# Optimization experiments

Hardware: AMD Instinct MI355X
Metric: run time of the kernel (lower is better)

The kernel has to match this reference:

```python
import jax, jax.numpy as jnp
import numpy as np

D = 2048
H = 16
HD = D // H
DFF = 8192
EPS = 1e-6


def rmsnorm(x, w):
    xf = x.astype(jnp.float32)
    var = jnp.mean(xf * xf, axis=-1, keepdims=True)
    return w * (xf * jax.lax.rsqrt(var + EPS)).astype(x.dtype)


def setup_inputs() -> dict:
    key = jax.random.key(0)
    ks = jax.random.split(key, 10)
    s = 0.02
    return {
        "hidden_states": jax.random.normal(ks[0], (2, 2048, D), jnp.float32),
        "wq": jax.random.normal(ks[1], (D, D), jnp.float32) * s,
        "wk": jax.random.normal(ks[2], (D, D), jnp.float32) * s,
        "wv": jax.random.normal(ks[3], (D, D), jnp.float32) * s,
        "wo": jax.random.normal(ks[4], (D, D), jnp.float32) * s,
        "w_gate": jax.random.normal(ks[5], (DFF, D), jnp.float32) * s,
        "w_up": jax.random.normal(ks[6], (DFF, D), jnp.float32) * s,
        "w_down": jax.random.normal(ks[7], (D, DFF), jnp.float32) * s,
        "ln1_w": jnp.ones((D,), jnp.float32),
        "ln2_w": jnp.ones((D,), jnp.float32),
    }


def reference(hidden_states, wq, wk, wv, wo, w_gate, w_up, w_down, ln1_w, ln2_w):
    B, S, _ = hidden_states.shape
    residual = hidden_states
    x = rmsnorm(hidden_states, ln1_w)
    # projections (torch Linear: y = x @ W.T), split heads -> [B,H,S,HD]
    q = (x @ wq.T).reshape(B, S, H, HD).transpose(0, 2, 1, 3)
    k = (x @ wk.T).reshape(B, S, H, HD).transpose(0, 2, 1, 3)
    v = (x @ wv.T).reshape(B, S, H, HD).transpose(0, 2, 1, 3)
    scores = jnp.einsum("bhqd,bhkd->bhqk", q, k) / np.sqrt(HD).astype(np.float32)
    causal = jnp.triu(jnp.ones((S, S), bool), k=1)  # True above diagonal -> masked
    scores = jnp.where(causal, -jnp.inf, scores)
    attn = jax.nn.softmax(scores, axis=-1)
    out = jnp.einsum("bhqk,bhkd->bhqd", attn, v)
    out = out.transpose(0, 2, 1, 3).reshape(B, S, D)
    out = out @ wo.T
    hidden = residual + out
    residual = hidden
    y = rmsnorm(hidden, ln2_w)
    gate = y @ w_gate.T
    up = y @ w_up.T
    mlp = (jax.nn.silu(gate) * up) @ w_down.T
    return residual + mlp
```

## Files before the change

kernel.cpp:

```cpp
#include <hip/hip_runtime.h>
#include <stdint.h>

#define D_MODEL 2048
#define NHEADS  16
#define HEADDIM 128
#define DFF     8192
#define BATCH   2
#define SEQ     2048
#define NTOK    (BATCH*SEQ)
#define EPS     1e-6f
#define QKV_RS  (3*D_MODEL)

typedef unsigned short u16;
typedef short  s16x8 __attribute__((ext_vector_type(8)));
typedef float  f32x4 __attribute__((ext_vector_type(4)));

__device__ __forceinline__ u16 f2bf(float f) {
  union { float f; uint32_t u; } v; v.f = f;
  uint32_t u = v.u;
  return (u16)((u + 0x7fffu + ((u >> 16) & 1u)) >> 16);
}
__device__ __forceinline__ float bf2f(u16 h) {
  union { uint32_t u; float f; } v; v.u = ((uint32_t)h) << 16;
  return v.f;
}

__device__ __forceinline__ void gload_lds16(const void* g, void* l) {
  __builtin_amdgcn_global_load_lds(
      (const __attribute__((address_space(1))) void*)g,
      (__attribute__((address_space(3))) void*)l, 16, 0, 0);
}

__device__ __forceinline__ f32x4 mfma16(s16x8 a, s16x8 b, f32x4 c) {
  return __builtin_amdgcn_mfma_f32_16x16x32_bf16(a, b, c, 0, 0, 0);
}

#define BAR()   asm volatile("s_barrier" ::: "memory")
#define LGK0()  asm volatile("s_waitcnt lgkmcnt(0)" ::: "memory")

__device__ __forceinline__ void cvt_one(const float* in, u16* out, int i) {
  float4 v = ((const float4*)in)[i];
  uint32_t lo = (uint32_t)f2bf(v.x) | ((uint32_t)f2bf(v.y) << 16);
  uint32_t hi = (uint32_t)f2bf(v.z) | ((uint32_t)f2bf(v.w) << 16);
  uint2 st; st.x = lo; st.y = hi;
  ((uint2*)out)[i] = st;
}

__global__ __launch_bounds__(256)
void cvt_kernel(const float* __restrict__ in, u16* __restrict__ out, int n4)
{
  int idx = blockIdx.x * 256 + threadIdx.x;
  int stride = gridDim.x * 256;
  for (int i = idx; i < n4; i += stride) cvt_one(in, out, i);
}

__global__ __launch_bounds__(256)
void cvt4_kernel(const float* __restrict__ a, const float* __restrict__ b,
                 const float* __restrict__ c, const float* __restrict__ d,
                 u16* __restrict__ oa, u16* __restrict__ ob,
                 u16* __restrict__ oc, u16* __restrict__ od, int n4)
{
  int idx = blockIdx.x * 256 + threadIdx.x;
  int stride = gridDim.x * 256;
  for (int i = idx; i < 4 * n4; i += stride) {
    int w = i / n4, j = i - w * n4;
    const float* s = (w == 0) ? a : (w == 1) ? b : (w == 2) ? c : d;
    u16* o = (w == 0) ? oa : (w == 1) ? ob : (w == 2) ? oc : od;
    cvt_one(s, o, j);
  }
}

__global__ __launch_bounds__(256)
void cvt2_kernel(const float* __restrict__ a, const float* __restrict__ b,
                 u16* __restrict__ oa, u16* __restrict__ ob, int n4)
{
  int idx = blockIdx.x * 256 + threadIdx.x;
  int stride = gridDim.x * 256;
  for (int i = idx; i < 2 * n4; i += stride) {
    int w = i / n4, j = i - w * n4;
    cvt_one(w ? b : a, w ? ob : oa, j);
  }
}

__global__ __launch_bounds__(256)
void rmsnorm_kernel(const float* __restrict__ x, const float* __restrict__ w,
                    u16* __restrict__ out)
{
  int row = blockIdx.x;
  int tid = threadIdx.x;
  const float4* xr = (const float4*)(x + (size_t)row * D_MODEL);
  float4 a = xr[tid];
  float4 b = xr[tid + 256];
  float ss = a.x*a.x + a.y*a.y + a.z*a.z + a.w*a.w
           + b.x*b.x + b.y*b.y + b.z*b.z + b.w*b.w;
#pragma unroll
  for (int o = 32; o > 0; o >>= 1) ss += __shfl_xor(ss, o);
  __shared__ float red[4];
  if ((tid & 63) == 0) red[tid >> 6] = ss;
  __syncthreads();
  float tot = red[0] + red[1] + red[2] + red[3];
  float sc = rsqrtf(tot * (1.0f / D_MODEL) + EPS);
  const float4* wr = (const float4*)w;
  float4 wa = wr[tid], wb = wr[tid + 256];
  u16* orow = out + (size_t)row * D_MODEL;
  uint2 s0, s1;
  s0.x = (uint32_t)f2bf(a.x*wa.x*sc) | ((uint32_t)f2bf(a.y*wa.y*sc) << 16);
  s0.y = (uint32_t)f2bf(a.z*wa.z*sc) | ((uint32_t)f2bf(a.w*wa.w*sc) << 16);
  s1.x = (uint32_t)f2bf(b.x*wb.x*sc) | ((uint32_t)f2bf(b.y*wb.y*sc) << 16);
  s1.y = (uint32_t)f2bf(b.z*wb.z*sc) | ((uint32_t)f2bf(b.w*wb.w*sc) << 16);
  ((uint2*)orow)[tid] = s0;
  ((uint2*)orow)[tid + 256] = s1;
}

#define BM 128
#define BN 128
#define BK 64

template<int EPI>
__global__ __launch_bounds__(256, 2)
void gemm_bt(const u16* __restrict__ A, const u16* __restrict__ B,
             void* __restrict__ Cout, const float* __restrict__ aux,
             int M, int N, int K)
{
  __shared__ u16 As[BM * BK];
  __shared__ u16 Bs[BN * BK];
  const int nbn = N / BN;
  int bid = blockIdx.x;
  int swz = (gridDim.x & 7) ? bid : ((bid & 7) * (gridDim.x >> 3) + (bid >> 3));
  const int bm = swz / nbn, bn = swz % nbn;
  const int m0 = bm * BM, n0 = bn * BN;
  const int tid = threadIdx.x;
  const int lane = tid & 63;
  const int wm = tid >> 7, wn = (tid >> 6) & 1;
  const int lr = lane & 15, lg = lane >> 4;

  f32x4 acc[4][4] = {};

  for (int k0 = 0; k0 < K; k0 += BK) {
#pragma unroll
    for (int i = 0; i < 4; ++i) {
      int c = i * 256 + tid;
      int row = c >> 3, cr = c & 7;
      int g = cr ^ (row & 7);
      gload_lds16(A + (size_t)(m0 + row) * K + k0 + (g << 3), &As[c * 8]);
      gload_lds16(B + (size_t)(n0 + row) * K + k0 + (g << 3), &Bs[c * 8]);
    }
    __syncthreads();
#pragma unroll
    for (int kk = 0; kk < BK; kk += 32) {
      s16x8 a[4], b[4];
#pragma unroll
      for (int m = 0; m < 4; ++m) {
        int row = wm * 64 + m * 16 + lr;
        int j = (kk >> 3) + lg;
        a[m] = *(const s16x8*)&As[row * BK + ((j ^ (row & 7)) << 3)];
      }
#pragma unroll
      for (int n = 0; n < 4; ++n) {
        int row = wn * 64 + n * 16 + lr;
        int j = (kk >> 3) + lg;
        b[n] = *(const s16x8*)&Bs[row * BK + ((j ^ (row & 7)) << 3)];
      }
#pragma unroll
      for (int m = 0; m < 4; ++m)
#pragma unroll
        for (int n = 0; n < 4; ++n)
          acc[m][n] = mfma16(a[m], b[n], acc[m][n]);
    }
    __syncthreads();
  }

#pragma unroll
  for (int m = 0; m < 4; ++m) {
#pragma unroll
    for (int n = 0; n < 4; ++n) {
      int col = n0 + wn * 64 + n * 16 + lr;
#pragma unroll
      for (int r = 0; r < 4; ++r) {
        int row = m0 + wm * 64 + m * 16 + lg * 4 + r;
        size_t idx = (size_t)row * N + col;
        float v = acc[m][n][r];
        if (EPI == 0) {
          ((u16*)Cout)[idx] = f2bf(v);
        } else if (EPI == 1) {
          float up = bf2f(((u16*)Cout)[idx]);
          float s = v / (1.0f + __expf(-v));
          ((u16*)Cout)[idx] = f2bf(s * up);
        } else if (EPI == 2) {
          ((float*)Cout)[idx] = aux[idx] + v;
        } else {
          ((float*)Cout)[idx] += v;
        }
      }
    }
  }
}

template<int EPI>
__global__ __launch_bounds__(512, 2)
void gemm256(const u16* __restrict__ A, const u16* __restrict__ B,
             void* __restrict__ Cout, const float* __restrict__ aux,
             int M, int N, int K)
{
  __shared__ u16 As[2][2][256 * 32];
  __shared__ u16 Bs[2][2][256 * 32];
  const int nbn = N >> 8;
  const int bm = blockIdx.x / nbn, bn = blockIdx.x % nbn;
  const int m0 = bm << 8, n0 = bn << 8;
  const int tid = threadIdx.x, lane = tid & 63;
  const int wid = tid >> 6;
  const int wm = wid >> 2, wn = wid & 3;
  const int lr = lane & 15, lg = lane >> 4;

  f32x4 acc[8][4] = {};

  auto stA = [&](int t, int kh) {
    const u16* src = A + (size_t)m0 * K + t * 64 + kh * 32;
    u16* dst = &As[t & 1][kh][0];
#pragma unroll
    for (int i = 0; i < 2; ++i) {
      int c = i * 512 + tid;
      int row = c >> 2, sl = c & 3;
      int g = sl ^ ((row >> 1) & 3);
      gload_lds16(src + (size_t)row * K + (g << 3), dst + (c << 3));
    }
  };
  auto stB = [&](int t, int kh) {
    const u16* src = B + (size_t)n0 * K + t * 64 + kh * 32;
    u16* dst = &Bs[t & 1][kh][0];
#pragma unroll
    for (int i = 0; i < 2; ++i) {
      int c = i * 512 + tid;
      int row = c >> 2, sl = c & 3;
      int g = sl ^ ((row >> 1) & 3);
      gload_lds16(src + (size_t)row * K + (g << 3), dst + (c << 3));
    }
  };
  auto rdA = [&](int t, int kh, int m) -> s16x8 {
    int row = wm * 128 + m * 16 + lr;
    int sl = lg ^ ((row >> 1) & 3);
    return *(const s16x8*)&As[t & 1][kh][row * 32 + (sl << 3)];
  };
  auto rdB = [&](int t, int kh, int n) -> s16x8 {
    int row = wn * 64 + n * 16 + lr;
    int sl = lg ^ ((row >> 1) & 3);
    return *(const s16x8*)&Bs[t & 1][kh][row * 32 + (sl << 3)];
  };

  const int nt = K >> 6;

  stA(0, 0); stB(0, 0);
  stA(0, 1); stB(0, 1);
  asm volatile("s_waitcnt vmcnt(4)" ::: "memory");
  BAR();

#pragma unroll 1
  for (int t = 0; t < nt; ++t) {
    const bool pf = (t + 1 < nt);
    s16x8 a[4], b[4];

    if (pf) stA(t + 1, 0);
#pragma unroll
    for (int n = 0; n < 4; ++n) b[n] = rdB(t, 0, n);
#pragma unroll
    for (int m = 0; m < 4; ++m) a[m] = rdA(t, 0, m);
    BAR(); LGK0();
    __builtin_amdgcn_s_setprio(1);
#pragma unroll
    for (int m = 0; m < 4; ++m)
#pragma unroll
      for (int n = 0; n < 4; ++n) acc[m][n] = mfma16(a[m], b[n], acc[m][n]);
    __builtin_amdgcn_s_setprio(0);
    BAR();

    if (pf) stB(t + 1, 0);
#pragma unroll
    for (int m = 0; m < 4; ++m) a[m] = rdA(t, 0, m + 4);
    BAR(); LGK0();
    __builtin_amdgcn_s_setprio(1);
#pragma unroll
    for (int m = 0; m < 4; ++m)
#pragma unroll
      for (int n = 0; n < 4; ++n) acc[m + 4][n] = mfma16(a[m], b[n], acc[m + 4][n]);
    __builtin_amdgcn_s_setprio(0);
    if (pf) asm volatile("s_waitcnt vmcnt(4)" ::: "memory");
    else    asm volatile("s_waitcnt vmcnt(0)" ::: "memory");
    BAR();

    if (pf) stA(t + 1, 1);
#pragma unroll
    for (int n = 0; n < 4; ++n) b[n] = rdB(t, 1, n);
#pragma unroll
    for (int m = 0; m < 4; ++m) a[m] = rdA(t, 1, m);
    BAR(); LGK0();
    __builtin_amdgcn_s_setprio(1);
#pragma unroll
    for (int m = 0; m < 4; ++m)
#pragma unroll
      for (int n = 0; n < 4; ++n) acc[m][n] = mfma16(a[m], b[n], acc[m][n]);
    __builtin_amdgcn_s_setprio(0);
    BAR();

    if (pf) stB(t + 1, 1);
#pragma unroll
    for (int m = 0; m < 4; ++m) a[m] = rdA(t, 1, m + 4);
    BAR(); LGK0();
    __builtin_amdgcn_s_setprio(1);
#pragma unroll
    for (int m = 0; m < 4; ++m)
#pragma unroll
      for (int n = 0; n < 4; ++n) acc[m + 4][n] = mfma16(a[m], b[n], acc[m + 4][n]);
    __builtin_amdgcn_s_setprio(0);
    if (pf) asm volatile("s_waitcnt vmcnt(4)" ::: "memory");
    BAR();
  }

#pragma unroll
  for (int m = 0; m < 8; ++m) {
#pragma unroll
    for (int n = 0; n < 4; ++n) {
      int col = n0 + wn * 64 + n * 16 + lr;
#pragma unroll
      for (int r = 0; r < 4; ++r) {
        int row = m0 + wm * 128 + m * 16 + lg * 4 + r;
        size_t idx = (size_t)row * N + col;
        float v = acc[m][n][r];
        if (EPI == 0) {
          ((u16*)Cout)[idx] = f2bf(v);
        } else if (EPI == 1) {
          float up = bf2f(((u16*)Cout)[idx]);
          float s = v / (1.0f + __expf(-v));
          ((u16*)Cout)[idx] = f2bf(s * up);
        } else if (EPI == 2) {
          ((float*)Cout)[idx] = aux[idx] + v;
        } else {
          ((float*)Cout)[idx] += v;
        }
      }
    }
  }
}

#define QBLK 128
#define KVBLK 64

__global__ __launch_bounds__(256, 2)
void attn_kernel(const u16* __restrict__ QKV, u16* __restrict__ O)
{
  __shared__ u16 Ks[2][KVBLK * HEADDIM];
  __shared__ u16 Vt[HEADDIM * KVBLK];
  __shared__ u16 Pw[4][32 * KVBLK];

  const int bid = blockIdx.x;
  const int q4 = bid & 15;
  const int h  = (bid >> 4) & (NHEADS - 1);
  const int b  = bid >> 8;
  const int qb = b ? q4 : 15 - q4;
  const int tid = threadIdx.x, lane = tid & 63, wid = tid >> 6;
  const int lr = lane & 15, lg = lane >> 4;
  const size_t tokbase = (size_t)b * SEQ;
  const int hoff = h * HEADDIM;
  const int qr0 = qb * QBLK + wid * 32;
  const int wq_max = qr0 + 31;
  const int nkb = (qb + 1) * (QBLK / KVBLK);
  const float scale = 0.08838834764831845f;

  s16x8 qf[2][4];
#pragma unroll
  for (int m = 0; m < 2; ++m)
#pragma unroll
    for (int c = 0; c < 4; ++c)
      qf[m][c] = *(const s16x8*)(QKV + (tokbase + qr0 + m * 16 + lr) * QKV_RS
                                 + hoff + c * 32 + lg * 8);

  f32x4 o_acc[2][8] = {};
  float m_run[2][4], l_run[2][4];
#pragma unroll
  for (int m = 0; m < 2; ++m)
#pragma unroll
    for (int r = 0; r < 4; ++r) { m_run[m][r] = -1e30f; l_run[m][r] = 0.0f; }

  s16x8 v0[2], v1[2];

  {
    const u16* kbase = QKV + tokbase * QKV_RS + D_MODEL + hoff;
#pragma unroll
    for (int it = 0; it < 4; ++it) {
      int c = it * 256 + tid;
      int row = c >> 4, cr = c & 15;
      int g = cr ^ (row & 7);
      gload_lds16(kbase + (size_t)row * QKV_RS + g * 8, &Ks[0][c * 8]);
    }
    const u16* vbase = QKV + tokbase * QKV_RS + 2 * D_MODEL + hoff;
#pragma unroll
    for (int i = 0; i < 2; ++i) {
      int pi = i * 256 + tid;
      int rp = pi >> 4, dc = pi & 15;
      const u16* vp = vbase + (size_t)(rp * 2) * QKV_RS + dc * 8;
      v0[i] = *(const s16x8*)vp;
      v1[i] = *(const s16x8*)(vp + QKV_RS);
    }
    uint32_t* vt = (uint32_t*)&Vt[0];
#pragma unroll
    for (int i = 0; i < 2; ++i) {
      int pi = i * 256 + tid;
      int rp = pi >> 4, dc = pi & 15;
      int k0 = rp * 2;
      int base = ((k0 >> 3) ^ (dc & 7)) * 4 + ((k0 >> 1) & 3);
#pragma unroll
      for (int j = 0; j < 8; ++j)
        vt[(dc * 8 + j) * (KVBLK / 2) + base] =
            (uint32_t)(u16)v0[i][j] | ((uint32_t)(u16)v1[i][j] << 16);
    }
  }
  __syncthreads();

  for (int kb = 0; kb < nkb; ++kb) {
    const int buf = kb & 1;
    const bool nb = (kb + 1 < nkb);

    if (nb) {
      const u16* kbase = QKV + (tokbase + (size_t)(kb + 1) * KVBLK) * QKV_RS + D_MODEL + hoff;
#pragma unroll
      for (int it = 0; it < 4; ++it) {
        int c = it * 256 + tid;
        int row = c >> 4, cr = c & 15;
        int g = cr ^ (row & 7);
        gload_lds16(kbase + (size_t)row * QKV_RS + g * 8, &Ks[buf ^ 1][c * 8]);
      }
      const u16* vbase = QKV + (tokbase + (size_t)(kb + 1) * KVBLK) * QKV_RS + 2 * D_MODEL + hoff;
#pragma unroll
      for (int i = 0; i < 2; ++i) {
        int pi = i * 256 + tid;
        int rp = pi >> 4, dc = pi & 15;
        const u16* vp = vbase + (size_t)(rp * 2) * QKV_RS + dc * 8;
        v0[i] = *(const s16x8*)vp;
        v1[i] = *(const s16x8*)(vp + QKV_RS);
      }
    }

    if (kb * KVBLK <= wq_max) {
      f32x4 s_acc[2][4] = {};
#pragma unroll
      for (int kk = 0; kk < 4; ++kk) {
        s16x8 kf[4];
#pragma unroll
        for (int n = 0; n < 4; ++n) {
          int row = n * 16 + lr;
          int ch = (kk * 4 + lg) ^ (row & 7);
          kf[n] = *(const s16x8*)&Ks[buf][row * HEADDIM + ch * 8];
        }
#pragma unroll
        for (int m = 0; m < 2; ++m)
#pragma unroll
          for (int n = 0; n < 4; ++n)
            s_acc[m][n] = mfma16(qf[m][kk], kf[n], s_acc[m][n]);
      }

#pragma unroll
      for (int m = 0; m < 2; ++m) {
        float tmax[4] = {-1e30f, -1e30f, -1e30f, -1e30f};
        float sv[4][4];
#pragma unroll
        for (int n = 0; n < 4; ++n) {
          int key = kb * KVBLK + n * 16 + lr;
#pragma unroll
          for (int r = 0; r < 4; ++r) {
            int q = qr0 + m * 16 + lg * 4 + r;
            float s = s_acc[m][n][r] * scale;
            if (key > q) s = -1e30f;
            sv[n][r] = s;
            tmax[r] = fmaxf(tmax[r], s);
          }
        }
#pragma unroll
        for (int o = 1; o < 16; o <<= 1)
#pragma unroll
          for (int r = 0; r < 4; ++r)
            tmax[r] = fmaxf(tmax[r], __shfl_xor(tmax[r], o));

        float pf[4], psum[4];
#pragma unroll
        for (int r = 0; r < 4; ++r) {
          float mn = fmaxf(m_run[m][r], tmax[r]);
          pf[r] = __expf(m_run[m][r] - mn);
          m_run[m][r] = mn;
          psum[r] = 0.0f;
        }
#pragma unroll
        for (int n = 0; n < 4; ++n) {
          int keyl = n * 16 + lr;
#pragma unroll
          for (int r = 0; r < 4; ++r) {
            float p = __expf(sv[n][r] - m_run[m][r]);
            psum[r] += p;
            int ql = m * 16 + lg * 4 + r;
            int ch = (keyl >> 3) ^ (ql & 7);
            Pw[wid][ql * KVBLK + ch * 8 + (keyl & 7)] = f2bf(p);
          }
        }
#pragma unroll
        for (int o = 1; o < 16; o <<= 1)
#pragma unroll
          for (int r = 0; r < 4; ++r)
            psum[r] += __shfl_xor(psum[r], o);
#pragma unroll
        for (int r = 0; r < 4; ++r)
          l_run[m][r] = l_run[m][r] * pf[r] + psum[r];
#pragma unroll
        for (int t = 0; t < 8; ++t)
#pragma unroll
          for (int r = 0; r < 4; ++r)
            o_acc[m][t][r] *= pf[r];
      }

#pragma unroll
      for (int kk = 0; kk < 2; ++kk) {
        s16x8 pa[2];
#pragma unroll
        for (int m = 0; m < 2; ++m) {
          int ql = m * 16 + lr;
          int ch = (kk * 4 + lg) ^ (ql & 7);
          pa[m] = *(const s16x8*)&Pw[wid][ql * KVBLK + ch * 8];
        }
#pragma unroll
        for (int t = 0; t < 8; ++t) {
          int d = t * 16 + lr;
          int ch = (kk * 4 + lg) ^ ((d >> 3) & 7);
          s16x8 vf = *(const s16x8*)&Vt[d * KVBLK + ch * 8];
#pragma unroll
          for (int m = 0; m < 2; ++m)
            o_acc[m][t] = mfma16(pa[m], vf, o_acc[m][t]);
        }
      }
    }

    __syncthreads();
    if (nb) {
      uint32_t* vt = (uint32_t*)&Vt[0];
#pragma unroll
      for (int i = 0; i < 2; ++i) {
        int pi = i * 256 + tid;
        int rp = pi >> 4, dc = pi & 15;
        int k0 = rp * 2;
        int base = ((k0 >> 3) ^ (dc & 7)) * 4 + ((k0 >> 1) & 3);
#pragma unroll
        for (int j = 0; j < 8; ++j)
          vt[(dc * 8 + j) * (KVBLK / 2) + base] =
              (uint32_t)(u16)v0[i][j] | ((uint32_t)(u16)v1[i][j] << 16);
      }
    }
    __syncthreads();
  }

#pragma unroll
  for (int m = 0; m < 2; ++m)
#pragma unroll
    for (int t = 0; t < 8; ++t)
#pragma unroll
      for (int r = 0; r < 4; ++r) {
        int q = qr0 + m * 16 + lg * 4 + r;
        O[(tokbase + q) * D_MODEL + hoff + t * 16 + lr] =
            f2bf(o_acc[m][t][r] / l_run[m][r]);
      }
}

extern "C" void kernel_launch(void* const* d_in, const int* in_sizes, int n_in,
                              void* d_out, int out_size, void* d_ws, size_t ws_size,
                              hipStream_t stream)
{
  const float* hidden = (const float*)d_in[0];
  const float* wq    = (const float*)d_in[1];
  const float* wk    = (const float*)d_in[2];
  const float* wv    = (const float*)d_in[3];
  const float* wo    = (const float*)d_in[4];
  const float* wgate = (const float*)d_in[5];
  const float* wup   = (const float*)d_in[6];
  const float* wdown = (const float*)d_in[7];
  const float* ln1   = (const float*)d_in[8];
  const float* ln2   = (const float*)d_in[9];
  float* out = (float*)d_out;

  const size_t TD = (size_t)NTOK * D_MODEL;
  const size_t DD = (size_t)D_MODEL * D_MODEL;
  const size_t FD = (size_t)DFF * D_MODEL;

  u16* XN  = (u16*)d_ws;
  u16* QKV = XN + TD;
  u16* AO  = QKV + 3 * TD;
  u16* WB  = AO + TD;
  u16* GU  = WB + FD;

  dim3 b256(256), b512(512);

  cvt4_kernel<<<dim3(2048), b256, 0, stream>>>(
      wq, wk, wv, wo, WB + 0 * DD, WB + 1 * DD, WB + 2 * DD, WB + 3 * DD,
      (int)(DD / 4));

  rmsnorm_kernel<<<dim3(NTOK), b256, 0, stream>>>(hidden, ln1, XN);

  gemm256<0><<<dim3(16 * 24), b512, 0, stream>>>(XN, WB, QKV, nullptr, NTOK, 3 * D_MODEL, D_MODEL);

  attn_kernel<<<dim3(BATCH * NHEADS * (SEQ / QBLK)), b256, 0, stream>>>(QKV, AO);

  gemm_bt<2><<<dim3(32 * 16), b256, 0, stream>>>(AO, WB + 3 * DD, out, hidden, NTOK, D_MODEL, D_MODEL);

  cvt2_kernel<<<dim3(4096), b256, 0, stream>>>(wgate, wup, WB, QKV, (int)(FD / 4));

  rmsnorm_kernel<<<dim3(NTOK), b256, 0, stream>>>(out, ln2, XN);

  gemm256<0><<<dim3(16 * 32), b512, 0, stream>>>(XN, QKV, GU, nullptr, NTOK, DFF, D_MODEL);
  gemm256<1><<<dim3(16 * 32), b512, 0, stream>>>(XN, WB, GU, nullptr, NTOK, DFF, D_MODEL);

  cvt_kernel<<<dim3(8192), b256, 0, stream>>>(wdown, QKV, (int)(FD / 4));

  gemm_bt<3><<<dim3(32 * 16), b256, 0, stream>>>(GU, QKV, out, nullptr, NTOK, D_MODEL, DFF);
}
```

Measured before the change: 964.8 us.

## Software-pipeline GEMM main loop with register double-buffering of LDS fragments

Restructures the 256x256 GEMM main loop so LDS fragment reads for the next sub-step are issued while the MFMAs for the current sub-step run. Fragments live in two register sets, global-to-LDS prefetch is split across half-tiles two steps ahead with clamped source indices, and the barrier count per K-tile drops from eight to two. The aim is to hide LDS latency and barrier stalls behind matrix-core work. In exchange it uses more registers and issues redundant loads at the tail, and the reduced barriers carry a risk of LDS read/write races.

```diff
diff --git a/kernel.cpp b/kernel.cpp
--- a/kernel.cpp
+++ b/kernel.cpp
@@ -214,9 +214,9 @@
 
   f32x4 acc[8][4] = {};
 
-  auto stA = [&](int t, int kh) {
-    const u16* src = A + (size_t)m0 * K + t * 64 + kh * 32;
-    u16* dst = &As[t & 1][kh][0];
+  auto stA = [&](int td, int ts, int kh) {
+    const u16* src = A + (size_t)m0 * K + ts * 64 + kh * 32;
+    u16* dst = &As[td & 1][kh][0];
 #pragma unroll
     for (int i = 0; i < 2; ++i) {
       int c = i * 512 + tid;
@@ -225,9 +225,9 @@
       gload_lds16(src + (size_t)row * K + (g << 3), dst + (c << 3));
     }
   };
-  auto stB = [&](int t, int kh) {
-    const u16* src = B + (size_t)n0 * K + t * 64 + kh * 32;
-    u16* dst = &Bs[t & 1][kh][0];
+  auto stB = [&](int td, int ts, int kh) {
+    const u16* src = B + (size_t)n0 * K + ts * 64 + kh * 32;
+    u16* dst = &Bs[td & 1][kh][0];
 #pragma unroll
     for (int i = 0; i < 2; ++i) {
       int c = i * 512 + tid;
@@ -249,71 +249,76 @@
 
   const int nt = K >> 6;
 
-  stA(0, 0); stB(0, 0);
-  stA(0, 1); stB(0, 1);
+  stA(0, 0, 0); stB(0, 0, 0);
+  stA(0, 0, 1); stB(0, 0, 1);
   asm volatile("s_waitcnt vmcnt(4)" ::: "memory");
   BAR();
 
+  s16x8 aA[4], aB[4], bA[4], bB[4];
+#pragma unroll
+  for (int n = 0; n < 4; ++n) bA[n] = rdB(0, 0, n);
+#pragma unroll
+  for (int m = 0; m < 4; ++m) aA[m] = rdA(0, 0, m);
+  stA(1, 1, 0); stB(1, 1, 0);
+  asm volatile("s_waitcnt vmcnt(4)" ::: "memory");
+  BAR();
+
 #pragma unroll 1
   for (int t = 0; t < nt; ++t) {
-    const bool pf = (t + 1 < nt);
-    s16x8 a[4], b[4];
-
-    if (pf) stA(t + 1, 0);
-#pragma unroll
-    for (int n = 0; n < 4; ++n) b[n] = rdB(t, 0, n);
-#pragma unroll
-    for (int m = 0; m < 4; ++m) a[m] = rdA(t, 0, m);
-    BAR(); LGK0();
+    const int tp1 = t + 1, tp2 = t + 2;
+    const int s1 = tp1 < nt ? tp1 : nt - 1;
+    const int s2 = tp2 < nt ? tp2 : nt - 1;
+
+    stA(tp1, s1, 1);
+#pragma unroll
+    for (int m = 0; m < 4; ++m) aB[m] = rdA(t, 0, m + 4);
     __builtin_amdgcn_s_setprio(1);
 #pragma unroll
     for (int m = 0; m < 4; ++m)
 #pragma unroll
-      for (int n = 0; n < 4; ++n) acc[m][n] = mfma16(a[m], b[n], acc[m][n]);
+      for (int n = 0; n < 4; ++n) acc[m][n] = mfma16(aA[m], bA[n], acc[m][n]);
     __builtin_amdgcn_s_setprio(0);
+
+    stB(tp1, s1, 1);
+#pragma unroll
+    for (int n = 0; n < 4; ++n) bB[n] = rdB(t, 1, n);
+#pragma unroll
+    for (int m = 0; m < 4; ++m) aA[m] = rdA(t, 1, m);
+    __builtin_amdgcn_s_setprio(1);
+#pragma unroll
+    for (int m = 0; m < 4; ++m)
+#pragma unroll
+      for (int n = 0; n < 4; ++n) acc[m + 4][n] = mfma16(aB[m], bA[n], acc[m + 4][n]);
+    __builtin_amdgcn_s_setprio(0);
+    asm volatile("s_waitcnt vmcnt(4)" ::: "memory");
     BAR();
 
-    if (pf) stB(t + 1, 0);
-#pragma unroll
-    for (int m = 0; m < 4; ++m) a[m] = rdA(t, 0, m + 4);
-    BAR(); LGK0();
+    stA(tp2, s2, 0);
+#pragma unroll
+    for (int m = 0; m < 4; ++m) aB[m] = rdA(t, 1, m + 4);
     __builtin_amdgcn_s_setprio(1);
 #pragma unroll
     for (int m = 0; m < 4; ++m)
 #pragma unroll
-      for (int n = 0; n < 4; ++n) acc[m + 4][n] = mfma16(a[m], b[n], acc[m + 4][n]);
+      for (int n = 0; n < 4; ++n) acc[m][n] = mfma16(aA[m], bB[n], acc[m][n]);
     __builtin_amdgcn_s_setprio(0);
-    if (pf) asm volatile("s_waitcnt vmcnt(4)" ::: "memory");
-    else    asm volatile("s_waitcnt vmcnt(0)" ::: "memory");
+
+    stB(tp2, s2, 0);
+#pragma unroll
+    for (int n = 0; n < 4; ++n) bA[n] = rdB(tp1, 0, n);
+#pragma unroll
+    for (int m = 0; m < 4; ++m) aA[m] = rdA(tp1, 0, m);
+    __builtin_amdgcn_s_setprio(1);
+#pragma unroll
+    for (int m = 0; m < 4; ++m)
+#pragma unroll
+      for (int n = 0; n < 4; ++n) acc[m + 4][n] = mfma16(aB[m], bB[n], acc[m + 4][n]);
+    __builtin_amdgcn_s_setprio(0);
+    asm volatile("s_waitcnt vmcnt(4)" ::: "memory");
     BAR();
-
-    if (pf) stA(t + 1, 1);
-#pragma unroll
-    for (int n = 0; n < 4; ++n) b[n] = rdB(t, 1, n);
-#pragma unroll
-    for (int m = 0; m < 4; ++m) a[m] = rdA(t, 1, m);
-    BAR(); LGK0();
-    __builtin_amdgcn_s_setprio(1);
-#pragma unroll
-    for (int m = 0; m < 4; ++m)
-#pragma unroll
-      for (int n = 0; n < 4; ++n) acc[m][n] = mfma16(a[m], b[n], acc[m][n]);
-    __builtin_amdgcn_s_setprio(0);
-    BAR();
-
-    if (pf) stB(t + 1, 1);
-#pragma unroll
-    for (int m = 0; m < 4; ++m) a[m] = rdA(t, 1, m + 4);
-    BAR(); LGK0();
-    __builtin_amdgcn_s_setprio(1);
-#pragma unroll
-    for (int m = 0; m < 4; ++m)
-#pragma unroll
-      for (int n = 0; n < 4; ++n) acc[m + 4][n] = mfma16(a[m], b[n], acc[m + 4][n]);
-    __builtin_amdgcn_s_setprio(0);
-    if (pf) asm volatile("s_waitcnt vmcnt(4)" ::: "memory");
-    BAR();
-  }
+  }
+
+  asm volatile("s_waitcnt vmcnt(0)" ::: "memory");
 
 #pragma unroll
   for (int m = 0; m < 8; ++m) {
```

Result: faster. 910.5 us (-5.6%).
